# Optimization experiments

Measured on AMD Instinct MI355X. Metric: run time of the kernel, lower is better.

## Reference

```python
import jax, jax.numpy as jnp
import numpy as np

B, L, D, H = 2, 2048, 1024, 16
DH = D // H  # 64
SIGMA = float(np.sqrt(DH))  # sigma=None, learnable_sigma=False -> sqrt(d_head)


def setup_inputs() -> dict:
    key = jax.random.key(0)
    ks = jax.random.split(key, 5)
    x = jax.random.normal(ks[0], (B, L, D), dtype=jnp.float32)
    # causal visibility mask (1 = visible, 0 = masked), [B,1,L,L]
    mask = jnp.broadcast_to(jnp.tril(jnp.ones((L, L), jnp.int32))[None, None], (B, 1, L, L))
    scale = 0.02
    W_q = jax.random.normal(ks[1], (D, D), dtype=jnp.float32) * scale
    W_k = jax.random.normal(ks[2], (D, D), dtype=jnp.float32) * scale
    W_v = jax.random.normal(ks[3], (D, D), dtype=jnp.float32) * scale
    W_o = jax.random.normal(ks[4], (D, D), dtype=jnp.float32) * scale
    return {"x": x, "mask": mask, "W_q": W_q, "W_k": W_k, "W_v": W_v, "W_o": W_o}


def _split_heads(t):
    # [B,L,D] -> [B,H,L,DH]
    b, l, _ = t.shape
    return t.reshape(b, l, H, DH).transpose(0, 2, 1, 3)


def reference(x, mask, W_q, W_k, W_v, W_o):
    # nn.Linear(bias=False): y = x @ W.T
    Qh = _split_heads(x @ W_q.T)  # [B,H,L,DH]
    Kh = _split_heads(x @ W_k.T)
    Vh = _split_heads(x @ W_v.T)
    # RBF scores: -||q-k||^2 / (2 sigma^2)
    q_norm2 = jnp.sum(Qh * Qh, axis=-1, keepdims=True)          # [B,H,L,1]
    k_norm2 = jnp.sum(Kh * Kh, axis=-1)[..., None, :]            # [B,H,1,L]
    dot_qk = jnp.einsum('bhqd,bhkd->bhqk', Qh, Kh)               # [B,H,L,L]
    dist2 = q_norm2 + k_norm2 - 2.0 * dot_qk
    scores = -dist2 / (2.0 * SIGMA * SIGMA)
    scores = jnp.where(mask == 0, -jnp.inf, scores)
    attn = jax.nn.softmax(scores, axis=-1)
    Oh = jnp.einsum('bhqk,bhkd->bhqd', attn, Vh)                 # [B,H,L,DH]
    O = Oh.transpose(0, 2, 1, 3).reshape(B, L, D)
    return O @ W_o.T
```

## Files before the change

### kernel.cpp

```cpp
#include <hip/hip_runtime.h>

#define L_SEQ  2048
#define D_MODEL 1024
#define NH 16
#define DHEAD 64
#define BATCH 2

typedef __attribute__((ext_vector_type(8))) short bf16x8;
typedef __attribute__((ext_vector_type(4))) float f32x4;

__device__ inline ushort f2bf(float f) {
  unsigned int u = __builtin_bit_cast(unsigned int, f);
  return (ushort)((u + 0x7FFFu + ((u >> 16) & 1u)) >> 16);
}
__device__ inline float bf2f(ushort u) {
  return __builtin_bit_cast(float, (unsigned int)u << 16);
}

__device__ __forceinline__ void gload_lds16(const void* g, void* l) {
  __builtin_amdgcn_global_load_lds(
      (const __attribute__((address_space(1))) void*)g,
      (__attribute__((address_space(3))) void*)l, 16, 0, 0);
}

#define PROJ8 524288
#define WSZ8  131072
__global__ __launch_bounds__(256) void cvt_all(const float* __restrict__ x,
                                               const float* __restrict__ w0,
                                               const float* __restrict__ w1,
                                               const float* __restrict__ w2,
                                               const float* __restrict__ w3,
                                               ushort* __restrict__ xb,
                                               ushort* __restrict__ ob0,
                                               ushort* __restrict__ ob1,
                                               ushort* __restrict__ ob2,
                                               ushort* __restrict__ ob3) {
  const int gid = blockIdx.x * 256 + threadIdx.x;
  const float* in; ushort* out; int off;
  if (gid < PROJ8) { in = x; out = xb; off = gid; }
  else {
    const int j = gid - PROJ8;
    const int seg = j / WSZ8;
    off = j - seg * WSZ8;
    switch (seg) {
      case 0: in = w0; out = ob0; break;
      case 1: in = w1; out = ob1; break;
      case 2: in = w2; out = ob2; break;
      default: in = w3; out = ob3; break;
    }
  }
  const float4* p = (const float4*)in + (size_t)off * 2;
  const float4 a = p[0], b = p[1];
  ushort4 lo, hi;
  lo.x = f2bf(a.x); lo.y = f2bf(a.y); lo.z = f2bf(a.z); lo.w = f2bf(a.w);
  hi.x = f2bf(b.x); hi.y = f2bf(b.y); hi.z = f2bf(b.z); hi.w = f2bf(b.w);
  ((ushort4*)out)[(size_t)off * 2] = lo;
  ((ushort4*)out)[(size_t)off * 2 + 1] = hi;
}

__global__ __launch_bounds__(512, 2) void gemm8p(const ushort* __restrict__ A,
    const ushort* __restrict__ W0, const ushort* __restrict__ W1,
    const ushort* __restrict__ W2, ushort* __restrict__ Qb,
    ushort* __restrict__ Kb, ushort* __restrict__ Vtb) {
  __shared__ ushort As[2][2][128][64];
  __shared__ ushort Bs[2][2][128][64];
  const int tid = threadIdx.x;
  const int wid = tid >> 6, l = tid & 63, lr = l & 15, lg = l >> 4;
  const int wr = wid >> 2, wc = wid & 3;

  const int bid = blockIdx.x;
  const int swz = (bid & 7) * 24 + (bid >> 3);
  const int mt = swz / 12, nt_ = swz % 12;
  const int m0g = mt * 256;
  const ushort* W = (nt_ < 4) ? W0 : (nt_ < 8) ? W1 : W2;
  ushort* outQK = (nt_ < 4) ? Qb : Kb;
  const int mode2 = (nt_ >= 8);
  const int ncol0 = (nt_ & 3) * 256;

  const int srow = tid >> 3;
  const int schunk = (tid & 7) ^ (srow & 7);
  const ushort* Ag = A + (size_t)(m0g + srow) * D_MODEL + schunk * 8;
  const ushort* Wg = W + (size_t)(ncol0 + srow) * D_MODEL + schunk * 8;
  ushort* AsL = &As[0][0][0][0] + tid * 8;
  ushort* BsL = &Bs[0][0][0][0] + tid * 8;

#define STG_A(sl, h, T2)                                                        \
  {                                                                             \
    gload_lds16(Ag + (size_t)((h) * 128) * D_MODEL + (T2) * 64,                 \
                AsL + (sl) * 16384 + (h) * 8192);                               \
    gload_lds16(Ag + (size_t)((h) * 128 + 64) * D_MODEL + (T2) * 64,            \
                AsL + (sl) * 16384 + (h) * 8192 + 4096);                        \
  }
#define STG_B(sl, h, T2)                                                        \
  {                                                                             \
    gload_lds16(Wg + (size_t)((h) * 128) * D_MODEL + (T2) * 64,                 \
                BsL + (sl) * 16384 + (h) * 8192);                               \
    gload_lds16(Wg + (size_t)((h) * 128 + 64) * D_MODEL + (T2) * 64,            \
                BsL + (sl) * 16384 + (h) * 8192 + 4096);                        \
  }

  STG_A(0, 0, 0); STG_A(0, 1, 0); STG_B(0, 0, 0); STG_B(0, 1, 0);

  f32x4 acc[8][4] = {};
  bf16x8 bfr[4][2];
  const int NT = D_MODEL / 64;

#define PHASE(q)                                                                \
  {                                                                             \
    bf16x8 af[2][2];                                                            \
    _Pragma("unroll") for (int m2 = 0; m2 < 2; ++m2)                            \
      _Pragma("unroll") for (int kk = 0; kk < 2; ++kk)                          \
        af[m2][kk] = *(const bf16x8*)&As[s][wr][((q) * 2 + m2) * 16 + lr]       \
                                           [((kk * 4 + lg) ^ (lr & 7)) * 8];    \
    if (T + 1 < NT) {                                                           \
      if ((q) == 1)      { STG_A(s ^ 1, 1, T + 1); }                            \
      else if ((q) == 2) { STG_B(s ^ 1, 0, T + 1); }                            \
      else               { STG_B(s ^ 1, 1, T + 1); }                            \
    }                                                                           \
    __builtin_amdgcn_s_barrier();                                               \
    __builtin_amdgcn_s_setprio(1);                                              \
    _Pragma("unroll") for (int m2 = 0; m2 < 2; ++m2)                            \
      _Pragma("unroll") for (int kk = 0; kk < 2; ++kk)                          \
        _Pragma("unroll") for (int n = 0; n < 4; ++n)                           \
          acc[(q) * 2 + m2][n] = __builtin_amdgcn_mfma_f32_16x16x32_bf16(       \
              af[m2][kk], bfr[n][kk], acc[(q) * 2 + m2][n], 0, 0, 0);           \
    __builtin_amdgcn_s_setprio(0);                                              \
    __builtin_amdgcn_s_barrier();                                               \
  }

  for (int T = 0; T < NT; ++T) {
    const int s = T & 1;
    {
      if (T + 1 < NT) {
        STG_A(s ^ 1, 0, T + 1);
        asm volatile("s_waitcnt vmcnt(2)" ::: "memory");
      } else {
        asm volatile("s_waitcnt vmcnt(0)" ::: "memory");
      }
      __builtin_amdgcn_s_barrier();
#pragma unroll
      for (int n = 0; n < 4; ++n)
#pragma unroll
        for (int kk = 0; kk < 2; ++kk)
          bfr[n][kk] = *(const bf16x8*)&Bs[s][wc >> 1][(wc & 1) * 64 + n * 16 + lr]
                                          [((kk * 4 + lg) ^ (lr & 7)) * 8];
      bf16x8 af[2][2];
#pragma unroll
      for (int m2 = 0; m2 < 2; ++m2)
#pragma unroll
        for (int kk = 0; kk < 2; ++kk)
          af[m2][kk] = *(const bf16x8*)&As[s][wr][m2 * 16 + lr]
                                          [((kk * 4 + lg) ^ (lr & 7)) * 8];
      __builtin_amdgcn_s_setprio(1);
#pragma unroll
      for (int m2 = 0; m2 < 2; ++m2)
#pragma unroll
        for (int kk = 0; kk < 2; ++kk)
#pragma unroll
          for (int n = 0; n < 4; ++n)
            acc[m2][n] = __builtin_amdgcn_mfma_f32_16x16x32_bf16(
                af[m2][kk], bfr[n][kk], acc[m2][n], 0, 0, 0);
      __builtin_amdgcn_s_setprio(0);
      __builtin_amdgcn_s_barrier();
    }
    PHASE(1)
    PHASE(2)
    PHASE(3)
  }
#undef PHASE
#undef STG_A
#undef STG_B

  const int h = (nt_ & 3) * 4 + wc;
  if (!mode2) {
#pragma unroll
    for (int m = 0; m < 8; ++m)
#pragma unroll
      for (int r = 0; r < 4; ++r) {
        const int grow = m0g + wr * 128 + m * 16 + lg * 4 + r;
        const int b = grow >> 11, ll = grow & (L_SEQ - 1);
        ushort* dst = outQK + ((size_t)(b * NH + h) * L_SEQ + ll) * DHEAD;
#pragma unroll
        for (int n = 0; n < 4; ++n) dst[n * 16 + lr] = f2bf(acc[m][n][r]);
      }
  } else {
#pragma unroll
    for (int m = 0; m < 8; ++m) {
      const int grow0 = m0g + wr * 128 + m * 16 + lg * 4;
      const int b = grow0 >> 11, ll = grow0 & (L_SEQ - 1);
#pragma unroll
      for (int n = 0; n < 4; ++n) {
        ushort4 v;
        v.x = f2bf(acc[m][n][0]); v.y = f2bf(acc[m][n][1]);
        v.z = f2bf(acc[m][n][2]); v.w = f2bf(acc[m][n][3]);
        *(ushort4*)(Vtb + ((size_t)(b * NH + h) * DHEAD + n * 16 + lr) * L_SEQ + ll) = v;
      }
    }
  }
}

__global__ __launch_bounds__(256) void gemm128(const ushort* __restrict__ A,
    const ushort* __restrict__ W0, float* __restrict__ of) {
  __shared__ ushort As[2][128][32];
  __shared__ ushort Bs[2][128][32];
  const int tid = threadIdx.x;
  const int w = tid >> 6, l = tid & 63, lr = l & 15, lg = l >> 4;
  const int wr = w >> 1, wc = w & 1;

  const int cpx = gridDim.x >> 3;
  const int swz = (blockIdx.x & 7) * cpx + (blockIdx.x >> 3);
  const int ntile = swz % 8;
  const int m0 = (swz / 8) * 128;
  const int n0 = ntile * 128;

  const int srow = tid >> 2;
  const int skc_sw = (tid & 3) ^ (srow & 3);
  const ushort* Ag = A + (size_t)(m0 + srow) * D_MODEL + skc_sw * 8;
  const ushort* Wg = W0 + (size_t)(n0 + srow) * D_MODEL + skc_sw * 8;

#define STAGE(buf, k0)                                                      \
  {                                                                         \
    gload_lds16(Ag + (k0), &As[buf][0][0] + tid * 8);                       \
    gload_lds16(Ag + (size_t)64 * D_MODEL + (k0), &As[buf][0][0] + 2048 + tid * 8); \
    gload_lds16(Wg + (k0), &Bs[buf][0][0] + tid * 8);                       \
    gload_lds16(Wg + (size_t)64 * D_MODEL + (k0), &Bs[buf][0][0] + 2048 + tid * 8); \
  }

  STAGE(0, 0);

  f32x4 acc[4][4] = {};
  const int NT = D_MODEL / 32;
  for (int t = 0; t < NT; ++t) {
    const int cur = t & 1;
    if (t + 1 < NT) {
      STAGE(cur ^ 1, (t + 1) * 32);
      asm volatile("s_waitcnt vmcnt(4)" ::: "memory");
    } else {
      asm volatile("s_waitcnt vmcnt(0)" ::: "memory");
    }
    __builtin_amdgcn_s_barrier();

    bf16x8 af[4], bfv[4];
#pragma unroll
    for (int i = 0; i < 4; ++i)
      af[i] = *(const bf16x8*)&As[cur][wr * 64 + i * 16 + lr][(lg ^ (lr & 3)) * 8];
#pragma unroll
    for (int j = 0; j < 4; ++j)
      bfv[j] = *(const bf16x8*)&Bs[cur][wc * 64 + j * 16 + lr][(lg ^ (lr & 3)) * 8];
#pragma unroll
    for (int i = 0; i < 4; ++i)
#pragma unroll
      for (int j = 0; j < 4; ++j)
        acc[i][j] = __builtin_amdgcn_mfma_f32_16x16x32_bf16(af[i], bfv[j], acc[i][j], 0, 0, 0);
    __syncthreads();
  }
#undef STAGE

#pragma unroll
  for (int i = 0; i < 4; ++i)
#pragma unroll
    for (int r = 0; r < 4; ++r) {
      const int m = m0 + wr * 64 + i * 16 + lg * 4 + r;
#pragma unroll
      for (int j = 0; j < 4; ++j)
        of[(size_t)m * D_MODEL + n0 + wc * 64 + j * 16 + lr] = acc[i][j][r];
    }
}

__global__ __launch_bounds__(256) void kn_bf16(const ushort* __restrict__ K,
                                               float* __restrict__ Kn) {
  const int i = blockIdx.x * 256 + threadIdx.x;
  const ushort4* p = (const ushort4*)(K + (size_t)i * DHEAD);
  float s = 0.f;
#pragma unroll
  for (int j = 0; j < 16; ++j) {
    const ushort4 v = p[j];
    const float a = bf2f(v.x), b = bf2f(v.y), c = bf2f(v.z), d = bf2f(v.w);
    s += a * a + b * b + c * c + d * d;
  }
  Kn[i] = s * 0.0078125f;
}

__global__ __launch_bounds__(512, 4) void attn_mfma3(const ushort* __restrict__ Q,
                                                     const ushort* __restrict__ K,
                                                     const ushort* __restrict__ Vt,
                                                     const float* __restrict__ Kexp,
                                                     ushort* __restrict__ Ob) {
  const int blk = blockIdx.x;
  const int qb = 15 - (blk >> 5);
  const int bh = blk & 31;
  const int tid = threadIdx.x;
  const int w = tid >> 6, l = tid & 63, lr = l & 15, lg = l >> 4;
  const int q0w = qb * 128 + w * 16;
  const int nt = 2 * qb + 2;
  const int tbw = q0w >> 6;

  __shared__ ushort Ks[2][64][64];
  __shared__ ushort Vs[2][64][64];
  __shared__ ushort P[8][16][70];

  const size_t ho = (size_t)bh * L_SEQ * DHEAD;
  const ushort* Qh = Q + ho;
  const ushort* Kh = K + ho;
  const ushort* Vh = Vt + ho;
  const float* KeB = Kexp + (size_t)bh * L_SEQ;

  const bf16x8 qf0 = *(const bf16x8*)(Qh + (size_t)(q0w + lr) * DHEAD + lg * 8);
  const bf16x8 qf1 = *(const bf16x8*)(Qh + (size_t)(q0w + lr) * DHEAD + 32 + lg * 8);

  const int srow = tid >> 3;
  const int scs = (tid & 7) ^ (srow & 7);
  const ushort* Kg = Kh + (size_t)srow * DHEAD + scs * 8;
  const ushort* Vg = Vh + (size_t)srow * L_SEQ + scs * 8;

  gload_lds16(Kg, &Ks[0][0][0] + tid * 8);
  gload_lds16(Vg, &Vs[0][0][0] + tid * 8);

  f32x4 oacc[4] = {};
  f32x4 lsacc = {};
  bf16x8 ones;
#pragma unroll
  for (int i = 0; i < 8; ++i) ones[i] = (short)0x3F80;

  for (int t = 0; t < nt; ++t) {
    const int cur = t & 1;
    if (t + 1 < nt) {
      const size_t kb2 = (size_t)(t + 1) * 64;
      gload_lds16(Kg + kb2 * DHEAD, &Ks[cur ^ 1][0][0] + tid * 8);
      gload_lds16(Vg + kb2, &Vs[cur ^ 1][0][0] + tid * 8);
      asm volatile("s_waitcnt vmcnt(2)" ::: "memory");
    } else {
      asm volatile("s_waitcnt vmcnt(0)" ::: "memory");
    }
    __builtin_amdgcn_s_barrier();

    const int kbase = t * 64;
    float ke[4];
#pragma unroll
    for (int nf = 0; nf < 4; ++nf) ke[nf] = KeB[kbase + nf * 16 + lr];
    const bool maskT = (t >= tbw);

    __builtin_amdgcn_s_setprio(1);
#pragma unroll
    for (int nf = 0; nf < 4; ++nf) {
      const int row = nf * 16 + lr;
      const bf16x8 kf0 = *(const bf16x8*)&Ks[cur][row][((lg) ^ (lr & 7)) * 8];
      const bf16x8 kf1 = *(const bf16x8*)&Ks[cur][row][((4 + lg) ^ (lr & 7)) * 8];
      f32x4 s = {0.f, 0.f, 0.f, 0.f};
      s = __builtin_amdgcn_mfma_f32_16x16x32_bf16(qf0, kf0, s, 0, 0, 0);
      s = __builtin_amdgcn_mfma_f32_16x16x32_bf16(qf1, kf1, s, 0, 0, 0);
      const int key = kbase + row;
      const float keh = ke[nf];
#pragma unroll
      for (int r = 0; r < 4; ++r) {
        float p = __expf(s[r] * 0.015625f - keh);
        if (maskT && key > q0w + lg * 4 + r) p = 0.f;
        P[w][lg * 4 + r][nf * 16 + lr] = f2bf(p);
      }
    }
    const bf16x8 p0 = *(const bf16x8*)&P[w][lr][lg * 8];
    const bf16x8 p1 = *(const bf16x8*)&P[w][lr][32 + lg * 8];
    lsacc = __builtin_amdgcn_mfma_f32_16x16x32_bf16(p0, ones, lsacc, 0, 0, 0);
    lsacc = __builtin_amdgcn_mfma_f32_16x16x32_bf16(p1, ones, lsacc, 0, 0, 0);
#pragma unroll
    for (int nf = 0; nf < 4; ++nf) {
      const int row = nf * 16 + lr;
      const bf16x8 vf0 = *(const bf16x8*)&Vs[cur][row][((lg) ^ (lr & 7)) * 8];
      const bf16x8 vf1 = *(const bf16x8*)&Vs[cur][row][((4 + lg) ^ (lr & 7)) * 8];
      oacc[nf] = __builtin_amdgcn_mfma_f32_16x16x32_bf16(p0, vf0, oacc[nf], 0, 0, 0);
      oacc[nf] = __builtin_amdgcn_mfma_f32_16x16x32_bf16(p1, vf1, oacc[nf], 0, 0, 0);
    }
    __builtin_amdgcn_s_setprio(0);
    __builtin_amdgcn_s_barrier();
  }

  const int b = bh >> 4, h = bh & 15;
#pragma unroll
  for (int r = 0; r < 4; ++r) {
    const float inv = 1.0f / lsacc[r];
    const int q = q0w + lg * 4 + r;
#pragma unroll
    for (int nf = 0; nf < 4; ++nf)
      Ob[((size_t)(b * L_SEQ + q)) * D_MODEL + h * DHEAD + nf * 16 + lr] =
          f2bf(oacc[nf][r] * inv);
  }
}

extern "C" void kernel_launch(void* const* d_in, const int* in_sizes, int n_in,
                              void* d_out, int out_size, void* d_ws, size_t ws_size,
                              hipStream_t stream) {
  const float* x  = (const float*)d_in[0];
  const float* Wq = (const float*)d_in[2];
  const float* Wk = (const float*)d_in[3];
  const float* Wv = (const float*)d_in[4];
  const float* Wo = (const float*)d_in[5];

  const size_t PROJ = (size_t)BATCH * L_SEQ * D_MODEL;
  const size_t WSZ  = (size_t)D_MODEL * D_MODEL;
  ushort* xb  = (ushort*)d_ws;
  ushort* Wqb = xb + PROJ;
  ushort* Wkb = Wqb + WSZ;
  ushort* Wvb = Wkb + WSZ;
  ushort* Wob = Wvb + WSZ;
  ushort* Qb  = Wob + WSZ;
  ushort* Kb  = Qb + PROJ;
  ushort* Vtb = Kb + PROJ;
  ushort* Obf = Vtb + PROJ;
  float*  Kn  = (float*)(Obf + PROJ);

  cvt_all<<<(PROJ8 + 4 * WSZ8) / 256, 256, 0, stream>>>(x, Wq, Wk, Wv, Wo,
                                                        xb, Wqb, Wkb, Wvb, Wob);
  gemm8p<<<192, 512, 0, stream>>>(xb, Wqb, Wkb, Wvb, Qb, Kb, Vtb);
  kn_bf16<<<BATCH * NH * L_SEQ / 256, 256, 0, stream>>>(Kb, Kn);
  attn_mfma3<<<BATCH * NH * (L_SEQ / 128), 512, 0, stream>>>(Qb, Kb, Vtb, Kn, Obf);
  gemm128<<<256, 256, 0, stream>>>(Obf, Wob, (float*)d_out);
}
```

Measured before the change: 133.9 us.

## Halve attention query tile to 64 rows with 4-wave blocks and prefetched key norms

Each attention block now handles 64 query rows with 4 waves instead of 128 rows with 8 waves. The grid doubles to 1024 blocks, causal work becomes finer grained and only the diagonal tile needs masking. K/V staging issues four 16-byte loads per thread, and the per-key norm values for the next tile are prefetched one iteration ahead. The exp argument is folded into an fma. In exchange, each K/V tile is loaded from global memory by twice as many blocks, and there are fewer waves per block to hide latency.

```diff
diff --git a/kernel.cpp b/kernel.cpp
--- a/kernel.cpp
+++ b/kernel.cpp
@@ -281,23 +281,22 @@
   Kn[i] = s * 0.0078125f;
 }
 
-__global__ __launch_bounds__(512, 4) void attn_mfma3(const ushort* __restrict__ Q,
+__global__ __launch_bounds__(256, 3) void attn_mfma4(const ushort* __restrict__ Q,
                                                      const ushort* __restrict__ K,
                                                      const ushort* __restrict__ Vt,
                                                      const float* __restrict__ Kexp,
                                                      ushort* __restrict__ Ob) {
   const int blk = blockIdx.x;
-  const int qb = 15 - (blk >> 5);
+  const int qb = 31 - (blk >> 5);
   const int bh = blk & 31;
   const int tid = threadIdx.x;
   const int w = tid >> 6, l = tid & 63, lr = l & 15, lg = l >> 4;
-  const int q0w = qb * 128 + w * 16;
-  const int nt = 2 * qb + 2;
-  const int tbw = q0w >> 6;
+  const int q0w = qb * 64 + w * 16;
+  const int nt = qb + 1;
 
   __shared__ ushort Ks[2][64][64];
   __shared__ ushort Vs[2][64][64];
-  __shared__ ushort P[8][16][70];
+  __shared__ ushort P[4][16][70];
 
   const size_t ho = (size_t)bh * L_SEQ * DHEAD;
   const ushort* Qh = Q + ho;
@@ -312,9 +311,21 @@
   const int scs = (tid & 7) ^ (srow & 7);
   const ushort* Kg = Kh + (size_t)srow * DHEAD + scs * 8;
   const ushort* Vg = Vh + (size_t)srow * L_SEQ + scs * 8;
-
-  gload_lds16(Kg, &Ks[0][0][0] + tid * 8);
-  gload_lds16(Vg, &Vs[0][0][0] + tid * 8);
+  const ushort* Kg2 = Kg + (size_t)32 * DHEAD;
+  const ushort* Vg2 = Vg + (size_t)32 * L_SEQ;
+
+#define STAGE_KV(buf, kb)                                                 \
+  {                                                                       \
+    gload_lds16(Kg + (size_t)(kb) * DHEAD, &Ks[buf][0][0] + tid * 8);     \
+    gload_lds16(Kg2 + (size_t)(kb) * DHEAD, &Ks[buf][32][0] + tid * 8);   \
+    gload_lds16(Vg + (kb), &Vs[buf][0][0] + tid * 8);                     \
+    gload_lds16(Vg2 + (kb), &Vs[buf][32][0] + tid * 8);                   \
+  }
+
+  float keC[4], keN[4] = {0.f, 0.f, 0.f, 0.f};
+#pragma unroll
+  for (int nf = 0; nf < 4; ++nf) keC[nf] = KeB[nf * 16 + lr];
+  STAGE_KV(0, 0);
 
   f32x4 oacc[4] = {};
   f32x4 lsacc = {};
@@ -325,20 +336,18 @@
   for (int t = 0; t < nt; ++t) {
     const int cur = t & 1;
     if (t + 1 < nt) {
-      const size_t kb2 = (size_t)(t + 1) * 64;
-      gload_lds16(Kg + kb2 * DHEAD, &Ks[cur ^ 1][0][0] + tid * 8);
-      gload_lds16(Vg + kb2, &Vs[cur ^ 1][0][0] + tid * 8);
-      asm volatile("s_waitcnt vmcnt(2)" ::: "memory");
+#pragma unroll
+      for (int nf = 0; nf < 4; ++nf) keN[nf] = KeB[(t + 1) * 64 + nf * 16 + lr];
+      asm volatile("" ::: "memory");
+      STAGE_KV(cur ^ 1, (size_t)(t + 1) * 64);
+      asm volatile("s_waitcnt vmcnt(4)" ::: "memory");
     } else {
       asm volatile("s_waitcnt vmcnt(0)" ::: "memory");
     }
     __builtin_amdgcn_s_barrier();
 
     const int kbase = t * 64;
-    float ke[4];
-#pragma unroll
-    for (int nf = 0; nf < 4; ++nf) ke[nf] = KeB[kbase + nf * 16 + lr];
-    const bool maskT = (t >= tbw);
+    const bool maskT = (t == qb);
 
     __builtin_amdgcn_s_setprio(1);
 #pragma unroll
@@ -350,10 +359,10 @@
       s = __builtin_amdgcn_mfma_f32_16x16x32_bf16(qf0, kf0, s, 0, 0, 0);
       s = __builtin_amdgcn_mfma_f32_16x16x32_bf16(qf1, kf1, s, 0, 0, 0);
       const int key = kbase + row;
-      const float keh = ke[nf];
+      const float keh = keC[nf];
 #pragma unroll
       for (int r = 0; r < 4; ++r) {
-        float p = __expf(s[r] * 0.015625f - keh);
+        float p = __expf(fmaf(s[r], 0.015625f, -keh));
         if (maskT && key > q0w + lg * 4 + r) p = 0.f;
         P[w][lg * 4 + r][nf * 16 + lr] = f2bf(p);
       }
@@ -372,7 +381,10 @@
     }
     __builtin_amdgcn_s_setprio(0);
     __builtin_amdgcn_s_barrier();
-  }
+#pragma unroll
+    for (int nf = 0; nf < 4; ++nf) keC[nf] = keN[nf];
+  }
+#undef STAGE_KV
 
   const int b = bh >> 4, h = bh & 15;
 #pragma unroll
@@ -412,6 +424,6 @@
                                                         xb, Wqb, Wkb, Wvb, Wob);
   gemm8p<<<192, 512, 0, stream>>>(xb, Wqb, Wkb, Wvb, Qb, Kb, Vtb);
   kn_bf16<<<BATCH * NH * L_SEQ / 256, 256, 0, stream>>>(Kb, Kn);
-  attn_mfma3<<<BATCH * NH * (L_SEQ / 128), 512, 0, stream>>>(Qb, Kb, Vtb, Kn, Obf);
+  attn_mfma4<<<BATCH * NH * (L_SEQ / 64), 256, 0, stream>>>(Qb, Kb, Vtb, Kn, Obf);
   gemm128<<<256, 256, 0, stream>>>(Obf, Wob, (float*)d_out);
 }
```

Result: faster. 122.6 us (-8.5%).
